# Kernel tuning notes

Measured on AMD Instinct MI355X. Metric: run time of the kernel, lower is better.

Reference implementation:

```python
import jax, jax.numpy as jnp
import numpy as np

B, S, E, H, I = 32, 257, 1024, 16, 4096
D = E // H  # head_dim = 64
EPS = 1e-5


def setup_inputs() -> dict:
    key = jax.random.key(0)
    ks = jax.random.split(key, 12)
    std = 0.02
    inp = {
        'hidden_states': jax.random.normal(ks[0], (B, S, E), jnp.float32),
        'attention_mask': jnp.zeros((B, 1, S, S), jnp.float32),
        'causal_attention_mask': jnp.zeros((B, 1, S, S), jnp.float32),
        'ln1_w': jnp.ones((E,), jnp.float32),
        'ln1_b': jnp.zeros((E,), jnp.float32),
        'q_w': jax.random.normal(ks[1], (E, E), jnp.float32) * std,
        'q_b': jnp.zeros((E,), jnp.float32),
        'k_w': jax.random.normal(ks[2], (E, E), jnp.float32) * std,
        'k_b': jnp.zeros((E,), jnp.float32),
        'v_w': jax.random.normal(ks[3], (E, E), jnp.float32) * std,
        'v_b': jnp.zeros((E,), jnp.float32),
        'o_w': jax.random.normal(ks[4], (E, E), jnp.float32) * std,
        'o_b': jnp.zeros((E,), jnp.float32),
        'ln2_w': jnp.ones((E,), jnp.float32),
        'ln2_b': jnp.zeros((E,), jnp.float32),
        'fc1_w': jax.random.normal(ks[5], (I, E), jnp.float32) * std,
        'fc1_b': jnp.zeros((I,), jnp.float32),
        'fc2_w': jax.random.normal(ks[6], (E, I), jnp.float32) * std,
        'fc2_b': jnp.zeros((E,), jnp.float32),
    }
    return inp


def _layernorm(x, w, b):
    mu = jnp.mean(x, axis=-1, keepdims=True)
    var = jnp.mean(jnp.square(x - mu), axis=-1, keepdims=True)
    return (x - mu) * jax.lax.rsqrt(var + EPS) * w + b


def _gelu_tanh(x):
    # 0.5*x*(1+tanh(sqrt(2/pi)*(x+0.044715*x^3)))
    c = np.sqrt(2.0 / np.pi).astype(np.float32)
    return 0.5 * x * (1.0 + jnp.tanh(c * (x + 0.044715 * x * x * x)))


def reference(hidden_states, attention_mask, causal_attention_mask,
              ln1_w, ln1_b, q_w, q_b, k_w, k_b, v_w, v_b, o_w, o_b,
              ln2_w, ln2_b, fc1_w, fc1_b, fc2_w, fc2_b):
    scale = D ** -0.5
    residual = hidden_states
    x = _layernorm(hidden_states, ln1_w, ln1_b)

    # projections (torch Linear: x @ W.T + b), q pre-scaled as in source
    q = (x @ q_w.T + q_b) * scale
    k = x @ k_w.T + k_b
    v = x @ v_w.T + v_b

    # [B, H, S, D]
    q = q.reshape(B, S, H, D).transpose(0, 2, 1, 3)
    k = k.reshape(B, S, H, D).transpose(0, 2, 1, 3)
    v = v.reshape(B, S, H, D).transpose(0, 2, 1, 3)

    scores = jnp.einsum('bhqd,bhkd->bhqk', q, k)  # [B,H,S,S]
    scores = scores + causal_attention_mask + attention_mask
    probs = jax.nn.softmax(scores, axis=-1)
    ctx = jnp.einsum('bhqk,bhkd->bhqd', probs, v)
    ctx = ctx.transpose(0, 2, 1, 3).reshape(B, S, E)
    attn_out = ctx @ o_w.T + o_b

    h = residual + attn_out
    residual = h
    x = _layernorm(h, ln2_w, ln2_b)
    x = _gelu_tanh(x @ fc1_w.T + fc1_b)
    x = x @ fc2_w.T + fc2_b
    return residual + x
```

## Files before the change

### kernel.cpp

```cpp
#include <hip/hip_runtime.h>

typedef unsigned short u16;
typedef unsigned int   u32;
typedef short s16x8 __attribute__((ext_vector_type(8)));
typedef float f32x4 __attribute__((ext_vector_type(4)));

#define MFMA16(A,B,C) __builtin_amdgcn_mfma_f32_16x16x32_bf16((A),(B),(C),0,0,0)
#define BAR()  asm volatile("s_barrier" ::: "memory")
#define LGKM0  asm volatile("s_waitcnt lgkmcnt(0)" ::: "memory")
#define VMC2   asm volatile("s_waitcnt vmcnt(2)" ::: "memory")
#define VMC0   asm volatile("s_waitcnt vmcnt(0)" ::: "memory")

#define B_   32
#define S_   257
#define E_   1024
#define H_   16
#define D_   64
#define I_   4096
#define M_   (B_*S_)

__device__ __forceinline__ u16 f2bf(float f) {
    u32 u = __float_as_uint(f);
    u32 r = u + 0x7fffu + ((u >> 16) & 1u);
    return (u16)(r >> 16);
}
__device__ __forceinline__ float bf2f(u16 b) {
    return __uint_as_float(((u32)b) << 16);
}

__device__ __forceinline__ void gload16(const void* g, void* l) {
    __builtin_amdgcn_global_load_lds(
        (const __attribute__((address_space(1))) u32*)g,
        (__attribute__((address_space(3))) u32*)l, 16, 0, 0);
}

__global__ __launch_bounds__(256)
void convert_w_kernel(const float* __restrict__ qw, const float* __restrict__ kw,
                      const float* __restrict__ vw, const float* __restrict__ ow,
                      const float* __restrict__ f1, const float* __restrict__ f2,
                      u16* __restrict__ dst)
{
    const int total4 = (12 * 1048576) / 4;
    for (int i = blockIdx.x * 256 + threadIdx.x; i < total4; i += gridDim.x * 256) {
        int e = i * 4;
        int seg = e >> 20;
        const float* srcp; int off;
        if (seg < 4)      { srcp = (seg == 0 ? qw : seg == 1 ? kw : seg == 2 ? vw : ow); off = e & 1048575; }
        else if (seg < 8) { srcp = f1; off = e - 4 * 1048576; }
        else              { srcp = f2; off = e - 8 * 1048576; }
        float4 v = *(const float4*)(srcp + off);
        ushort4 o;
        o.x = f2bf(v.x); o.y = f2bf(v.y); o.z = f2bf(v.z); o.w = f2bf(v.w);
        *(ushort4*)(dst + e) = o;
    }
}

__global__ __launch_bounds__(256)
void mask_combine_kernel(const float* __restrict__ am, const float* __restrict__ cm,
                         u16* __restrict__ msum)
{
    const int total = B_ * S_ * 272;
    for (int i = blockIdx.x * 256 + threadIdx.x; i < total; i += gridDim.x * 256) {
        int skv = i % 272;
        int rem = i / 272;
        int sq  = rem % S_;
        int b   = rem / S_;
        float v;
        if (skv < S_) {
            size_t o = ((size_t)b * S_ + sq) * S_ + skv;
            v = am[o] + cm[o];
        } else v = -1e30f;
        msum[i] = f2bf(v);
    }
}

__global__ __launch_bounds__(256)
void ln_kernel(const float* __restrict__ src, const float* __restrict__ gam,
               const float* __restrict__ bet, u16* __restrict__ dst)
{
    int row = blockIdx.x;
    const float4* p = (const float4*)(src + (size_t)row * E_);
    float4 x = p[threadIdx.x];
    float s  = x.x + x.y + x.z + x.w;
    float s2 = x.x * x.x + x.y * x.y + x.z * x.z + x.w * x.w;
#pragma unroll
    for (int xm = 1; xm < 64; xm <<= 1) {
        s  += __shfl_xor(s,  xm, 64);
        s2 += __shfl_xor(s2, xm, 64);
    }
    __shared__ float red[8];
    int wv = threadIdx.x >> 6;
    if ((threadIdx.x & 63) == 0) { red[wv] = s; red[4 + wv] = s2; }
    __syncthreads();
    s  = red[0] + red[1] + red[2] + red[3];
    s2 = red[4] + red[5] + red[6] + red[7];
    float mu  = s * (1.0f / 1024.0f);
    float var = s2 * (1.0f / 1024.0f) - mu * mu;
    float rs  = rsqrtf(var + 1e-5f);
    float4 g  = ((const float4*)gam)[threadIdx.x];
    float4 be = ((const float4*)bet)[threadIdx.x];
    ushort4 o;
    o.x = f2bf((x.x - mu) * rs * g.x + be.x);
    o.y = f2bf((x.y - mu) * rs * g.y + be.y);
    o.z = f2bf((x.z - mu) * rs * g.z + be.z);
    o.w = f2bf((x.w - mu) * rs * g.w + be.w);
    ((ushort4*)dst)[(size_t)row * 256 + threadIdx.x] = o;
}

template<int MODE>
__global__ __launch_bounds__(512, 2)
void gemm8(const u16* __restrict__ A,
           const u16* __restrict__ Bq, const u16* __restrict__ Bk, const u16* __restrict__ Bv,
           const float* __restrict__ biasq, const float* __restrict__ biask, const float* __restrict__ biasvv,
           const float* __restrict__ res, float* __restrict__ outF, float* __restrict__ outF1,
           u16* __restrict__ outBq, u16* __restrict__ outBk, u16* __restrict__ outBv,
           int M, int N, int Ks, int klen)
{
    __shared__ u16 lds[2][4][8192];
    const int tid = threadIdx.x, lane = tid & 63, w = tid >> 6;
    const int lr = lane & 15, lg = lane >> 4;
    const int wm = w >> 2, wn = w & 3;

    const u16* Bm = Bq; const float* bias = biasq; u16* outB = outBq;
    float scl = 1.0f; int nt = blockIdx.x; int k0 = 0; float* outP = outF;
    if (MODE == 0) {
        int mat = nt >> 2; nt &= 3;
        if (mat == 1)      { Bm = Bk; bias = biask; outB = outBk; }
        else if (mat == 2) { Bm = Bv; bias = biasvv; outB = outBv; }
        if (mat == 0) scl = 0.125f;
    } else if (MODE == 3) {
        int kz = nt & 1; nt >>= 1;
        k0 = kz * klen;
        if (kz) outP = outF1;
    }
    const int m0 = blockIdx.y * 256, n0 = nt * 256;
    const int NT = klen >> 6, NI = klen >> 7;
    const int tb = k0 >> 6;

    {
    }
    const int p    = w * 1024 + lane * 16;
    const int lby  = p ^ (((p >> 7) & 7) << 4);
    const int srow = lby >> 7;
    const int scol = (lby & 127) >> 1;

    auto STAGE = [&](int buf, int half, const u16* src, int grow0, int rowmax, int t) {
#pragma unroll
        for (int s = 0; s < 2; ++s) {
            int gr = grow0 + s * 64 + srow; if (gr > rowmax) gr = rowmax;
            gload16(src + (size_t)gr * Ks + ((tb + t) << 6) + scol,
                    (char*)&lds[buf][half][0] + s * 8192 + w * 1024);
        }
    };
    auto LDA = [&](int buf, int mh, int mf, int kh) -> s16x8 {
        const char* b = (const char*)&lds[buf][wm][0];
        int inrow = mh * 64 + mf * 16 + lr;
        return *(const s16x8*)(b + inrow * 128 + ((kh * 64 + lg * 16) ^ ((lr & 7) << 4)));
    };
    auto LDB = [&](int buf, int nh, int nf, int kh) -> s16x8 {
        const char* b = (const char*)&lds[buf][2 + (wn >> 1)][0];
        int inrow = (wn & 1) * 64 + nh * 32 + nf * 16 + lr;
        return *(const s16x8*)(b + inrow * 128 + ((kh * 64 + lg * 16) ^ ((lr & 7) << 4)));
    };

    f32x4 acc[8][4];
#pragma unroll
    for (int i = 0; i < 8; ++i)
#pragma unroll
        for (int j = 0; j < 4; ++j) { f32x4 z = {0.f, 0.f, 0.f, 0.f}; acc[i][j] = z; }

    s16x8 a[4][2], b[2][2][2];
    auto MFQ = [&](int mh, int nh) {
        __builtin_amdgcn_s_setprio(1);
#pragma unroll
        for (int mf = 0; mf < 4; ++mf)
#pragma unroll
            for (int nf = 0; nf < 2; ++nf)
#pragma unroll
                for (int kh = 0; kh < 2; ++kh)
                    acc[mh * 4 + mf][nh * 2 + nf] =
                        MFMA16(a[mf][kh], b[nh][nf][kh], acc[mh * 4 + mf][nh * 2 + nf]);
        __builtin_amdgcn_s_setprio(0);
    };

    STAGE(0, 0, A,  m0,       M - 1, 0);
    STAGE(0, 1, A,  m0 + 128, M - 1, 0);
    STAGE(0, 2, Bm, n0,       N - 1, 0);
    STAGE(0, 3, Bm, n0 + 128, N - 1, 0);
    STAGE(1, 0, A,  m0,       M - 1, 1);
    VMC2;
    BAR();

    for (int i = 0; i < NI; ++i) {
        const int t1 = 2 * i + 1, t2 = 2 * i + 2, t3 = 2 * i + 3;
        const bool more = (i + 1 < NI);
#pragma unroll
        for (int mf = 0; mf < 4; ++mf)
#pragma unroll
            for (int kh = 0; kh < 2; ++kh) a[mf][kh] = LDA(0, 0, mf, kh);
#pragma unroll
        for (int nf = 0; nf < 2; ++nf)
#pragma unroll
            for (int kh = 0; kh < 2; ++kh) b[0][nf][kh] = LDB(0, 0, nf, kh);
        STAGE(1, 1, A, m0 + 128, M - 1, t1);
        BAR(); LGKM0;
        MFQ(0, 0);
        BAR();
#pragma unroll
        for (int nf = 0; nf < 2; ++nf)
#pragma unroll
            for (int kh = 0; kh < 2; ++kh) b[1][nf][kh] = LDB(0, 1, nf, kh);
        STAGE(1, 2, Bm, n0, N - 1, t1);
        BAR(); LGKM0;
        MFQ(0, 1);
        BAR();
#pragma unroll
        for (int mf = 0; mf < 4; ++mf)
#pragma unroll
            for (int kh = 0; kh < 2; ++kh) a[mf][kh] = LDA(0, 1, mf, kh);
        STAGE(1, 3, Bm, n0 + 128, N - 1, t1);
        BAR(); LGKM0;
        MFQ(1, 1);
        BAR();
        if (more) STAGE(0, 0, A, m0, M - 1, t2);
        MFQ(1, 0);
        if (more) { VMC2; } else { VMC0; }
        BAR();
#pragma unroll
        for (int mf = 0; mf < 4; ++mf)
#pragma unroll
            for (int kh = 0; kh < 2; ++kh) a[mf][kh] = LDA(1, 0, mf, kh);
#pragma unroll
        for (int nf = 0; nf < 2; ++nf)
#pragma unroll
            for (int kh = 0; kh < 2; ++kh) b[0][nf][kh] = LDB(1, 0, nf, kh);
        if (more) STAGE(0, 2, Bm, n0, N - 1, t2);
        BAR(); LGKM0;
        MFQ(0, 0);
        BAR();
#pragma unroll
        for (int nf = 0; nf < 2; ++nf)
#pragma unroll
            for (int kh = 0; kh < 2; ++kh) b[1][nf][kh] = LDB(1, 1, nf, kh);
        if (more) STAGE(0, 3, Bm, n0 + 128, N - 1, t2);
        BAR(); LGKM0;
        MFQ(0, 1);
        BAR();
#pragma unroll
        for (int mf = 0; mf < 4; ++mf)
#pragma unroll
            for (int kh = 0; kh < 2; ++kh) a[mf][kh] = LDA(1, 1, mf, kh);
        if (more) STAGE(0, 1, A, m0 + 128, M - 1, t2);
        BAR(); LGKM0;
        MFQ(1, 1);
        BAR();
        if (more) STAGE(1, 0, A, m0, M - 1, t3);
        MFQ(1, 0);
        if (more) VMC2;
        BAR();
    }

    float biasv[4];
    if (MODE != 3) {
#pragma unroll
        for (int an = 0; an < 4; ++an)
            biasv[an] = bias[n0 + wn * 64 + (an >> 1) * 32 + (an & 1) * 16 + lr];
    }
#pragma unroll
    for (int am = 0; am < 8; ++am) {
#pragma unroll
        for (int r = 0; r < 4; ++r) {
            int row = m0 + wm * 128 + (am >> 2) * 64 + (am & 3) * 16 + lg * 4 + r;
            if (row >= M) continue;
            if (MODE == 0) {
                int bb = row / S_;
                int ss = row - bb * S_;
#pragma unroll
                for (int an = 0; an < 4; ++an) {
                    int col = n0 + wn * 64 + (an >> 1) * 32 + (an & 1) * 16 + lr;
                    int hh = col >> 6, dd = col & 63;
                    float v = (acc[am][an][r] + biasv[an]) * scl;
                    outB[(((size_t)bb * H_ + hh) * S_ + ss) * D_ + dd] = f2bf(v);
                }
            } else if (MODE == 1) {
                size_t base = (size_t)row * N;
#pragma unroll
                for (int an = 0; an < 4; ++an) {
                    int col = n0 + wn * 64 + (an >> 1) * 32 + (an & 1) * 16 + lr;
                    outF[base + col] = acc[am][an][r] + biasv[an] + res[base + col];
                }
            } else if (MODE == 2) {
                size_t base = (size_t)row * N;
#pragma unroll
                for (int an = 0; an < 4; ++an) {
                    int col = n0 + wn * 64 + (an >> 1) * 32 + (an & 1) * 16 + lr;
                    float x = acc[am][an][r] + biasv[an];
                    float u = 0.7978845608028654f * (x + 0.044715f * x * x * x);
                    float t = tanhf(u);
                    outB[base + col] = f2bf(0.5f * x * (1.0f + t));
                }
            } else {
                size_t base = (size_t)row * N;
#pragma unroll
                for (int an = 0; an < 4; ++an) {
                    int col = n0 + wn * 64 + (an >> 1) * 32 + (an & 1) * 16 + lr;
                    outP[base + col] = acc[am][an][r];
                }
            }
        }
    }
}

__global__ __launch_bounds__(256)
void fc2_reduce(const float* __restrict__ P0, const float* __restrict__ P1,
                const float* __restrict__ res, const float* __restrict__ bias,
                float* __restrict__ out)
{
    const int n4 = (M_ * E_) / 4;
    for (int i = blockIdx.x * 256 + threadIdx.x; i < n4; i += gridDim.x * 256) {
        float4 x0 = ((const float4*)P0)[i];
        float4 x1 = ((const float4*)P1)[i];
        float4 rr = ((const float4*)res)[i];
        float4 bb = ((const float4*)bias)[i & 255];
        float4 o;
        o.x = x0.x + x1.x + rr.x + bb.x;
        o.y = x0.y + x1.y + rr.y + bb.y;
        o.z = x0.z + x1.z + rr.z + bb.z;
        o.w = x0.w + x1.w + rr.w + bb.w;
        ((float4*)out)[i] = o;
    }
}

__global__ __launch_bounds__(256)
void attn_kernel(const u16* __restrict__ qg_, const u16* __restrict__ kg_,
                 const u16* __restrict__ vg_, const u16* __restrict__ msum,
                 u16* __restrict__ ctx)
{
    __shared__ u16 Ks[272 * 72];
    __shared__ u16 Vt[64 * 296];
    __shared__ u16 Ps[4][16 * 32];
    const int bh = blockIdx.x;
    const int b = bh >> 4, hh = bh & 15;
    const u16* kg = kg_ + (size_t)bh * (S_ * D_);
    const u16* vg = vg_ + (size_t)bh * (S_ * D_);
    const u16* qg = qg_ + (size_t)bh * (S_ * D_);
    const int tid = threadIdx.x, lane = tid & 63, wv = tid >> 6;

    for (int c = tid; c < (S_ * D_) / 8; c += 256) {
        int s = c >> 3, d8 = (c & 7) << 3;
        s16x8 val = *(const s16x8*)(kg + s * 64 + d8);
        *(s16x8*)&Ks[s * 72 + d8] = val;
    }
    for (int idx = tid; idx < 15 * 64; idx += 256) {
        int rr = 257 + (idx >> 6), cc = idx & 63;
        Ks[rr * 72 + cc] = 0;
    }
    for (int c = tid; c < (S_ * D_) / 8; c += 256) {
        int s = c >> 3, d8 = (c & 7) << 3;
        s16x8 val = *(const s16x8*)(vg + s * 64 + d8);
#pragma unroll
        for (int j = 0; j < 8; ++j) Vt[(d8 + j) * 296 + s] = (u16)val[j];
    }
    for (int idx = tid; idx < 64 * 39; idx += 256) {
        int dd = idx / 39, cc = 257 + idx % 39;
        Vt[dd * 296 + cc] = 0;
    }
    __syncthreads();

    const int lr = lane & 15, lg = lane >> 4;
    for (int qb = wv; qb < 17; qb += 4) {
        const int q0 = qb * 16;
        int qrow = q0 + lr; if (qrow > S_ - 1) qrow = S_ - 1;
        s16x8 aq0 = *(const s16x8*)(qg + qrow * 64 + lg * 8);
        s16x8 aq1 = *(const s16x8*)(qg + qrow * 64 + 32 + lg * 8);

        f32x4 sc[17];
#pragma unroll
        for (int t = 0; t < 17; ++t) { f32x4 z = {0.f, 0.f, 0.f, 0.f}; sc[t] = z; }
#pragma unroll
        for (int t = 0; t < 17; ++t) {
            s16x8 b0 = *(const s16x8*)&Ks[(t * 16 + lr) * 72 + lg * 8];
            s16x8 b1 = *(const s16x8*)&Ks[(t * 16 + lr) * 72 + 32 + lg * 8];
            sc[t] = MFMA16(aq0, b0, sc[t]);
            sc[t] = MFMA16(aq1, b1, sc[t]);
        }
        float mx[4] = {-3e38f, -3e38f, -3e38f, -3e38f};
#pragma unroll
        for (int r = 0; r < 4; ++r) {
            int sq = q0 + lg * 4 + r; if (sq > S_ - 1) sq = S_ - 1;
            const u16* mrow = msum + ((size_t)b * S_ + sq) * 272;
#pragma unroll
            for (int t = 0; t < 17; ++t) {
                sc[t][r] += bf2f(mrow[t * 16 + lr]);
                mx[r] = fmaxf(mx[r], sc[t][r]);
            }
        }
#pragma unroll
        for (int r = 0; r < 4; ++r) {
#pragma unroll
            for (int xm = 1; xm <= 8; xm <<= 1)
                mx[r] = fmaxf(mx[r], __shfl_xor(mx[r], xm, 64));
        }
        float sum[4] = {0.f, 0.f, 0.f, 0.f};
#pragma unroll
        for (int t = 0; t < 17; ++t)
#pragma unroll
            for (int r = 0; r < 4; ++r) {
                float e = __expf(sc[t][r] - mx[r]);
                sc[t][r] = e; sum[r] += e;
            }
#pragma unroll
        for (int r = 0; r < 4; ++r) {
#pragma unroll
            for (int xm = 1; xm <= 8; xm <<= 1)
                sum[r] += __shfl_xor(sum[r], xm, 64);
        }

        f32x4 ac[4];
#pragma unroll
        for (int nt = 0; nt < 4; ++nt) { f32x4 z = {0.f, 0.f, 0.f, 0.f}; ac[nt] = z; }
        u16* myP = &Ps[wv][0];
#pragma unroll
        for (int kc = 0; kc < 9; ++kc) {
#pragma unroll
            for (int tt = 0; tt < 2; ++tt) {
                const int t = kc * 2 + tt;
#pragma unroll
                for (int r = 0; r < 4; ++r) {
                    float pv = (t < 17) ? sc[(t < 17) ? t : 0][r] : 0.f;
                    myP[(lg * 4 + r) * 32 + tt * 16 + lr] = f2bf(pv);
                }
            }
            s16x8 pa = *(const s16x8*)&myP[lr * 32 + lg * 8];
#pragma unroll
            for (int nt = 0; nt < 4; ++nt) {
                s16x8 bv = *(const s16x8*)&Vt[(nt * 16 + lr) * 296 + kc * 32 + lg * 8];
                ac[nt] = MFMA16(pa, bv, ac[nt]);
            }
        }
#pragma unroll
        for (int r = 0; r < 4; ++r) {
            int sq = q0 + lg * 4 + r;
            if (sq < S_) {
                float rd = 1.0f / sum[r];
                size_t base = (((size_t)b * S_ + sq) * H_ + hh) * D_;
#pragma unroll
                for (int nt = 0; nt < 4; ++nt)
                    ctx[base + nt * 16 + lr] = f2bf(ac[nt][r] * rd);
            }
        }
    }
}

extern "C" void kernel_launch(void* const* d_in, const int* in_sizes, int n_in,
                              void* d_out, int out_size, void* d_ws, size_t ws_size,
                              hipStream_t stream)
{
    const float* hid   = (const float*)d_in[0];
    const float* am    = (const float*)d_in[1];
    const float* cm    = (const float*)d_in[2];
    const float* ln1w  = (const float*)d_in[3];
    const float* ln1b  = (const float*)d_in[4];
    const float* qw    = (const float*)d_in[5];
    const float* qbias = (const float*)d_in[6];
    const float* kw    = (const float*)d_in[7];
    const float* kbias = (const float*)d_in[8];
    const float* vw    = (const float*)d_in[9];
    const float* vbias = (const float*)d_in[10];
    const float* ow    = (const float*)d_in[11];
    const float* obias = (const float*)d_in[12];
    const float* ln2w  = (const float*)d_in[13];
    const float* ln2b  = (const float*)d_in[14];
    const float* f1w   = (const float*)d_in[15];
    const float* f1b   = (const float*)d_in[16];
    const float* f2w   = (const float*)d_in[17];
    const float* f2b   = (const float*)d_in[18];
    float* out = (float*)d_out;

    const size_t ME = (size_t)M_ * E_;
    u16* Wq   = (u16*)d_ws;
    u16* Wk   = Wq + 1048576;
    u16* Wv   = Wk + 1048576;
    u16* Wo   = Wv + 1048576;
    u16* Wf1  = Wo + 1048576;
    u16* Wf2  = Wf1 + 4 * 1048576;
    u16* xln  = Wf2 + 4 * 1048576;
    u16* qb_  = xln + ME;
    u16* kb_  = qb_ + ME;
    u16* vb_  = kb_ + ME;
    u16* ctx  = vb_ + ME;
    float* hbuf = (float*)(ctx + ME);
    u16* msum = (u16*)(hbuf + ME);
    u16* act  = qb_;
    u16* x2   = xln;
    float* P0 = (float*)(msum + (size_t)B_ * S_ * 272);
    float* P1 = P0 + ME;
    const size_t need = (size_t)((char*)(P1 + ME) - (char*)d_ws);
    const bool split = ws_size >= need;

    convert_w_kernel<<<3072, 256, 0, stream>>>(qw, kw, vw, ow, f1w, f2w, Wq);
    mask_combine_kernel<<<8736, 256, 0, stream>>>(am, cm, msum);
    ln_kernel<<<M_, 256, 0, stream>>>(hid, ln1w, ln1b, xln);
    gemm8<0><<<dim3(12, 33), 512, 0, stream>>>(xln, Wq, Wk, Wv, qbias, kbias, vbias,
                                               nullptr, nullptr, nullptr, qb_, kb_, vb_,
                                               M_, 1024, 1024, 1024);
    attn_kernel<<<512, 256, 0, stream>>>(qb_, kb_, vb_, msum, ctx);
    gemm8<1><<<dim3(4, 33), 512, 0, stream>>>(ctx, Wo, nullptr, nullptr, obias, nullptr, nullptr,
                                              hid, hbuf, nullptr, nullptr, nullptr, nullptr,
                                              M_, 1024, 1024, 1024);
    ln_kernel<<<M_, 256, 0, stream>>>(hbuf, ln2w, ln2b, x2);
    gemm8<2><<<dim3(16, 33), 512, 0, stream>>>(x2, Wf1, nullptr, nullptr, f1b, nullptr, nullptr,
                                               nullptr, nullptr, nullptr, act, nullptr, nullptr,
                                               M_, 4096, 1024, 1024);
    if (split) {
        gemm8<3><<<dim3(8, 33), 512, 0, stream>>>(act, Wf2, nullptr, nullptr, nullptr, nullptr, nullptr,
                                                  nullptr, P0, P1, nullptr, nullptr, nullptr,
                                                  M_, 1024, 4096, 2048);
        fc2_reduce<<<2048, 256, 0, stream>>>(P0, P1, hbuf, f2b, out);
    } else {
        gemm8<1><<<dim3(4, 33), 512, 0, stream>>>(act, Wf2, nullptr, nullptr, f2b, nullptr, nullptr,
                                                  hbuf, out, nullptr, nullptr, nullptr, nullptr,
                                                  M_, 1024, 4096, 4096);
    }
}
```

Baseline: 451.2 us.

## Simplify GEMM main loop to double-buffered tiles, split-K out-proj, exp-based GELU

Replaces the hand-interleaved 8-phase GEMM loop with a plain double-buffered loop. Each iteration loads the whole K-tile's fragments, runs all MFMAs, then prefetches tile t+2, keeping two tiles in flight with vmcnt(8). The out-projection now uses split-K with two partial buffers and a reduce kernel, which doubles the block count at the cost of extra fp32 traffic. GELU's tanh is rewritten as the sigmoid form x*e^u/(1+e^u) using __expf, which is cheaper than tanhf. The simpler loop gives up the fine-grained overlap of LDS reads with MFMA and the setprio hints.

```diff
diff --git a/kernel.cpp b/kernel.cpp
--- a/kernel.cpp
+++ b/kernel.cpp
@@ -7,8 +7,7 @@
 
 #define MFMA16(A,B,C) __builtin_amdgcn_mfma_f32_16x16x32_bf16((A),(B),(C),0,0,0)
 #define BAR()  asm volatile("s_barrier" ::: "memory")
-#define LGKM0  asm volatile("s_waitcnt lgkmcnt(0)" ::: "memory")
-#define VMC2   asm volatile("s_waitcnt vmcnt(2)" ::: "memory")
+#define VMC8   asm volatile("s_waitcnt vmcnt(8)" ::: "memory")
 #define VMC0   asm volatile("s_waitcnt vmcnt(0)" ::: "memory")
 
 #define B_   32
@@ -109,7 +108,7 @@
 
 template<int MODE>
 __global__ __launch_bounds__(512, 2)
-void gemm8(const u16* __restrict__ A,
+void gemmK(const u16* __restrict__ A,
            const u16* __restrict__ Bq, const u16* __restrict__ Bk, const u16* __restrict__ Bv,
            const float* __restrict__ biasq, const float* __restrict__ biask, const float* __restrict__ biasvv,
            const float* __restrict__ res, float* __restrict__ outF, float* __restrict__ outF1,
@@ -134,23 +133,27 @@
         if (kz) outP = outF1;
     }
     const int m0 = blockIdx.y * 256, n0 = nt * 256;
-    const int NT = klen >> 6, NI = klen >> 7;
-    const int tb = k0 >> 6;
-
-    {
-    }
+    const int NTt = klen >> 6;
+    const int tb  = k0 >> 6;
+
     const int p    = w * 1024 + lane * 16;
     const int lby  = p ^ (((p >> 7) & 7) << 4);
     const int srow = lby >> 7;
     const int scol = (lby & 127) >> 1;
 
-    auto STAGE = [&](int buf, int half, const u16* src, int grow0, int rowmax, int t) {
+    auto STAGEH = [&](int buf, int half, const u16* src, int grow0, int rowmax, int t) {
 #pragma unroll
         for (int s = 0; s < 2; ++s) {
             int gr = grow0 + s * 64 + srow; if (gr > rowmax) gr = rowmax;
             gload16(src + (size_t)gr * Ks + ((tb + t) << 6) + scol,
                     (char*)&lds[buf][half][0] + s * 8192 + w * 1024);
         }
+    };
+    auto STAGE4 = [&](int buf, int t) {
+        STAGEH(buf, 0, A,  m0,       M - 1, t);
+        STAGEH(buf, 1, A,  m0 + 128, M - 1, t);
+        STAGEH(buf, 2, Bm, n0,       N - 1, t);
+        STAGEH(buf, 3, Bm, n0 + 128, N - 1, t);
     };
     auto LDA = [&](int buf, int mh, int mf, int kh) -> s16x8 {
         const char* b = (const char*)&lds[buf][wm][0];
@@ -169,94 +172,45 @@
 #pragma unroll
         for (int j = 0; j < 4; ++j) { f32x4 z = {0.f, 0.f, 0.f, 0.f}; acc[i][j] = z; }
 
-    s16x8 a[4][2], b[2][2][2];
-    auto MFQ = [&](int mh, int nh) {
-        __builtin_amdgcn_s_setprio(1);
-#pragma unroll
-        for (int mf = 0; mf < 4; ++mf)
+    STAGE4(0, 0);
+    STAGE4(1, 1);
+    VMC8;
+    BAR();
+
+    for (int t = 0; t < NTt; ++t) {
+        const int cur = t & 1;
+        s16x8 bf[2][2][2];
+#pragma unroll
+        for (int nh = 0; nh < 2; ++nh)
 #pragma unroll
             for (int nf = 0; nf < 2; ++nf)
 #pragma unroll
                 for (int kh = 0; kh < 2; ++kh)
-                    acc[mh * 4 + mf][nh * 2 + nf] =
-                        MFMA16(a[mf][kh], b[nh][nf][kh], acc[mh * 4 + mf][nh * 2 + nf]);
-        __builtin_amdgcn_s_setprio(0);
-    };
-
-    STAGE(0, 0, A,  m0,       M - 1, 0);
-    STAGE(0, 1, A,  m0 + 128, M - 1, 0);
-    STAGE(0, 2, Bm, n0,       N - 1, 0);
-    STAGE(0, 3, Bm, n0 + 128, N - 1, 0);
-    STAGE(1, 0, A,  m0,       M - 1, 1);
-    VMC2;
-    BAR();
-
-    for (int i = 0; i < NI; ++i) {
-        const int t1 = 2 * i + 1, t2 = 2 * i + 2, t3 = 2 * i + 3;
-        const bool more = (i + 1 < NI);
-#pragma unroll
-        for (int mf = 0; mf < 4; ++mf)
-#pragma unroll
-            for (int kh = 0; kh < 2; ++kh) a[mf][kh] = LDA(0, 0, mf, kh);
-#pragma unroll
-        for (int nf = 0; nf < 2; ++nf)
-#pragma unroll
-            for (int kh = 0; kh < 2; ++kh) b[0][nf][kh] = LDB(0, 0, nf, kh);
-        STAGE(1, 1, A, m0 + 128, M - 1, t1);
-        BAR(); LGKM0;
-        MFQ(0, 0);
+                    bf[nh][nf][kh] = LDB(cur, nh, nf, kh);
+#pragma unroll
+        for (int mh = 0; mh < 2; ++mh) {
+            s16x8 af[4][2];
+#pragma unroll
+            for (int mf = 0; mf < 4; ++mf)
+#pragma unroll
+                for (int kh = 0; kh < 2; ++kh)
+                    af[mf][kh] = LDA(cur, mh, mf, kh);
+#pragma unroll
+            for (int mf = 0; mf < 4; ++mf)
+#pragma unroll
+                for (int nh = 0; nh < 2; ++nh)
+#pragma unroll
+                    for (int nf = 0; nf < 2; ++nf)
+#pragma unroll
+                        for (int kh = 0; kh < 2; ++kh)
+                            acc[mh * 4 + mf][nh * 2 + nf] =
+                                MFMA16(af[mf][kh], bf[nh][nf][kh], acc[mh * 4 + mf][nh * 2 + nf]);
+        }
         BAR();
-#pragma unroll
-        for (int nf = 0; nf < 2; ++nf)
-#pragma unroll
-            for (int kh = 0; kh < 2; ++kh) b[1][nf][kh] = LDB(0, 1, nf, kh);
-        STAGE(1, 2, Bm, n0, N - 1, t1);
-        BAR(); LGKM0;
-        MFQ(0, 1);
-        BAR();
-#pragma unroll
-        for (int mf = 0; mf < 4; ++mf)
-#pragma unroll
-            for (int kh = 0; kh < 2; ++kh) a[mf][kh] = LDA(0, 1, mf, kh);
-        STAGE(1, 3, Bm, n0 + 128, N - 1, t1);
-        BAR(); LGKM0;
-        MFQ(1, 1);
-        BAR();
-        if (more) STAGE(0, 0, A, m0, M - 1, t2);
-        MFQ(1, 0);
-        if (more) { VMC2; } else { VMC0; }
-        BAR();
-#pragma unroll
-        for (int mf = 0; mf < 4; ++mf)
-#pragma unroll
-            for (int kh = 0; kh < 2; ++kh) a[mf][kh] = LDA(1, 0, mf, kh);
-#pragma unroll
-        for (int nf = 0; nf < 2; ++nf)
-#pragma unroll
-            for (int kh = 0; kh < 2; ++kh) b[0][nf][kh] = LDB(1, 0, nf, kh);
-        if (more) STAGE(0, 2, Bm, n0, N - 1, t2);
-        BAR(); LGKM0;
-        MFQ(0, 0);
-        BAR();
-#pragma unroll
-        for (int nf = 0; nf < 2; ++nf)
-#pragma unroll
-            for (int kh = 0; kh < 2; ++kh) b[1][nf][kh] = LDB(1, 1, nf, kh);
-        if (more) STAGE(0, 3, Bm, n0 + 128, N - 1, t2);
-        BAR(); LGKM0;
-        MFQ(0, 1);
-        BAR();
-#pragma unroll
-        for (int mf = 0; mf < 4; ++mf)
-#pragma unroll
-            for (int kh = 0; kh < 2; ++kh) a[mf][kh] = LDA(1, 1, mf, kh);
-        if (more) STAGE(0, 1, A, m0 + 128, M - 1, t2);
-        BAR(); LGKM0;
-        MFQ(1, 1);
-        BAR();
-        if (more) STAGE(1, 0, A, m0, M - 1, t3);
-        MFQ(1, 0);
-        if (more) VMC2;
+        if (t + 2 < NTt) STAGE4(cur, t + 2);
+        if (t + 1 < NTt) {
+            if (t + 2 < NTt) { VMC8; } else { VMC0; }
+        }
         BAR();
     }
 
@@ -295,9 +249,10 @@
                 for (int an = 0; an < 4; ++an) {
                     int col = n0 + wn * 64 + (an >> 1) * 32 + (an & 1) * 16 + lr;
                     float x = acc[am][an][r] + biasv[an];
-                    float u = 0.7978845608028654f * (x + 0.044715f * x * x * x);
-                    float t = tanhf(u);
-                    outB[base + col] = f2bf(0.5f * x * (1.0f + t));
+                    float u2 = 1.5957691216057308f * (x + 0.044715f * x * x * x);
+                    u2 = fminf(u2, 80.0f);
+                    float tt = __expf(u2);
+                    outB[base + col] = f2bf(x * tt / (1.0f + tt));
                 }
             } else {
                 size_t base = (size_t)row * N;
@@ -312,9 +267,9 @@
 }
 
 __global__ __launch_bounds__(256)
-void fc2_reduce(const float* __restrict__ P0, const float* __restrict__ P1,
-                const float* __restrict__ res, const float* __restrict__ bias,
-                float* __restrict__ out)
+void splitk_reduce(const float* __restrict__ P0, const float* __restrict__ P1,
+                   const float* __restrict__ res, const float* __restrict__ bias,
+                   float* __restrict__ out)
 {
     const int n4 = (M_ * E_) / 4;
     for (int i = blockIdx.x * 256 + threadIdx.x; i < n4; i += gridDim.x * 256) {
@@ -501,24 +456,31 @@
     convert_w_kernel<<<3072, 256, 0, stream>>>(qw, kw, vw, ow, f1w, f2w, Wq);
     mask_combine_kernel<<<8736, 256, 0, stream>>>(am, cm, msum);
     ln_kernel<<<M_, 256, 0, stream>>>(hid, ln1w, ln1b, xln);
-    gemm8<0><<<dim3(12, 33), 512, 0, stream>>>(xln, Wq, Wk, Wv, qbias, kbias, vbias,
+    gemmK<0><<<dim3(12, 33), 512, 0, stream>>>(xln, Wq, Wk, Wv, qbias, kbias, vbias,
                                                nullptr, nullptr, nullptr, qb_, kb_, vb_,
                                                M_, 1024, 1024, 1024);
     attn_kernel<<<512, 256, 0, stream>>>(qb_, kb_, vb_, msum, ctx);
-    gemm8<1><<<dim3(4, 33), 512, 0, stream>>>(ctx, Wo, nullptr, nullptr, obias, nullptr, nullptr,
-                                              hid, hbuf, nullptr, nullptr, nullptr, nullptr,
-                                              M_, 1024, 1024, 1024);
+    if (split) {
+        gemmK<3><<<dim3(8, 33), 512, 0, stream>>>(ctx, Wo, nullptr, nullptr, nullptr, nullptr, nullptr,
+                                                  nullptr, P0, P1, nullptr, nullptr, nullptr,
+                                                  M_, 1024, 1024, 512);
+        splitk_reduce<<<2048, 256, 0, stream>>>(P0, P1, hid, obias, hbuf);
+    } else {
+        gemmK<1><<<dim3(4, 33), 512, 0, stream>>>(ctx, Wo, nullptr, nullptr, obias, nullptr, nullptr,
+                                                  hid, hbuf, nullptr, nullptr, nullptr, nullptr,
+                                                  M_, 1024, 1024, 1024);
+    }
     ln_kernel<<<M_, 256, 0, stream>>>(hbuf, ln2w, ln2b, x2);
-    gemm8<2><<<dim3(16, 33), 512, 0, stream>>>(x2, Wf1, nullptr, nullptr, f1b, nullptr, nullptr,
+    gemmK<2><<<dim3(16, 33), 512, 0, stream>>>(x2, Wf1, nullptr, nullptr, f1b, nullptr, nullptr,
                                                nullptr, nullptr, nullptr, act, nullptr, nullptr,
                                                M_, 4096, 1024, 1024);
     if (split) {
-        gemm8<3><<<dim3(8, 33), 512, 0, stream>>>(act, Wf2, nullptr, nullptr, nullptr, nullptr, nullptr,
+        gemmK<3><<<dim3(8, 33), 512, 0, stream>>>(act, Wf2, nullptr, nullptr, nullptr, nullptr, nullptr,
                                                   nullptr, P0, P1, nullptr, nullptr, nullptr,
                                                   M_, 1024, 4096, 2048);
-        fc2_reduce<<<2048, 256, 0, stream>>>(P0, P1, hbuf, f2b, out);
+        splitk_reduce<<<2048, 256, 0, stream>>>(P0, P1, hbuf, f2b, out);
     } else {
-        gemm8<1><<<dim3(4, 33), 512, 0, stream>>>(act, Wf2, nullptr, nullptr, f2b, nullptr, nullptr,
+        gemmK<1><<<dim3(4, 33), 512, 0, stream>>>(act, Wf2, nullptr, nullptr, f2b, nullptr, nullptr,
                                                   hbuf, out, nullptr, nullptr, nullptr, nullptr,
                                                   M_, 1024, 4096, 4096);
     }
```

New measurement: 451.8 us. Within noise of the previous version (+0.1%).
